# Kernel optimization log

Measured on AMD Instinct MI355X. Metric: run time of the kernel, lower is better.

## Reference

```python
import jax, jax.numpy as jnp
import numpy as np

CH = 256
HEADS = 4
RED = 8  # SE reduction on 2*CH channels


def _conv2d(x, w, pad):
    # x: [b,c,h,w], w: [o,i,kh,kw]
    return jax.lax.conv_general_dilated(
        x, w, window_strides=(1, 1), padding=[(pad, pad), (pad, pad)],
        dimension_numbers=('NCHW', 'OIHW', 'NCHW'))


def setup_inputs() -> dict:
    key = jax.random.key(0)
    ks = jax.random.split(key, 12)
    b, c, h, w = 4, CH, 64, 64
    c2 = 2 * c
    s = 0.02
    inp = {
        'color_feat': jax.random.normal(ks[0], (b, c, h, w), jnp.float32),
        'gray_feat': jax.random.normal(ks[1], (b, c, h, w), jnp.float32),
        'Wq': jax.random.normal(ks[2], (c, c), jnp.float32) * s,
        'Wk': jax.random.normal(ks[3], (c, c), jnp.float32) * s,
        'Wv': jax.random.normal(ks[4], (c, c), jnp.float32) * s,
        'Wproj': jax.random.normal(ks[5], (c, c), jnp.float32) * s,
        'ca_w1': jax.random.normal(ks[6], (c2 // RED, c2), jnp.float32) * s,
        'ca_w2': jax.random.normal(ks[7], (c2, c2 // RED), jnp.float32) * s,
        'sa_w': jax.random.normal(ks[8], (1, 2, 7, 7), jnp.float32) * s,
        'fuse_w': jax.random.normal(ks[9], (c, c2, 3, 3), jnp.float32) * s,
        'bn_gamma': jnp.ones((c,), jnp.float32),
        'bn_beta': jnp.zeros((c,), jnp.float32),
        'bn_mean': jnp.zeros((c,), jnp.float32),
        'bn_var': jnp.ones((c,), jnp.float32),
    }
    return inp


def reference(color_feat, gray_feat, Wq, Wk, Wv, Wproj, ca_w1, ca_w2,
              sa_w, fuse_w, bn_gamma, bn_beta, bn_mean, bn_var):
    b, c, h, w = color_feat.shape
    nh = HEADS
    d = c // nh
    scale = d ** -0.5

    def heads(x, W):
        # 1x1 conv then split heads: [b,c,h,w] -> [b,nh,hw,d]
        y = jnp.einsum('bchw,oc->bohw', x, W)
        return y.reshape(b, nh, d, h * w).transpose(0, 1, 3, 2)

    q = heads(color_feat, Wq)
    k = heads(gray_feat, Wk)
    v = heads(gray_feat, Wv)

    attn = jax.nn.softmax(jnp.einsum('bnid,bnjd->bnij', q, k) * scale, axis=-1)
    out = jnp.einsum('bnij,bnjd->bnid', attn, v)
    out = out.transpose(0, 1, 3, 2).reshape(b, c, h, w)
    out = jnp.einsum('bchw,oc->bohw', out, Wproj)

    cat = jnp.concatenate([out, gray_feat], axis=1)  # [b,2c,h,w]

    # Channel attention (SE with shared MLP on avg- and max-pooled vectors)
    def mlp(z):
        return jax.nn.relu(z @ ca_w1.T) @ ca_w2.T
    avg = cat.mean(axis=(2, 3))
    mx = cat.max(axis=(2, 3))
    wch = jax.nn.sigmoid(mlp(avg) + mlp(mx))[:, :, None, None]
    cat = cat * wch

    # Spatial attention: channel-mean/max -> 7x7 conv -> sigmoid gate
    sa_in = jnp.stack([cat.mean(axis=1), cat.max(axis=1)], axis=1)  # [b,2,h,w]
    wsp = jax.nn.sigmoid(_conv2d(sa_in, sa_w, pad=3))
    cat = cat * wsp

    # Fuse: 3x3 conv -> BatchNorm (inference stats) -> LeakyReLU(0.2)
    y = _conv2d(cat, fuse_w, pad=1)
    inv = bn_gamma / jnp.sqrt(bn_var + 1e-5)
    y = (y - bn_mean[None, :, None, None]) * inv[None, :, None, None] + bn_beta[None, :, None, None]
    return jnp.where(y > 0, y, 0.2 * y)
```

## Files before the change

kernel.cpp:

```cpp
#include <hip/hip_runtime.h>
#include <hip/hip_bf16.h>
#include <stdint.h>

#define HW_ 4096

typedef short bf16x8 __attribute__((ext_vector_type(8)));
typedef short short4v __attribute__((ext_vector_type(4)));
typedef short short8v __attribute__((ext_vector_type(8)));
typedef float f32x4 __attribute__((ext_vector_type(4)));
typedef float f32x16 __attribute__((ext_vector_type(16)));
typedef uint32_t u32x4 __attribute__((ext_vector_type(4)));

__device__ inline unsigned short f2bf(float x) {
  uint32_t u = __builtin_bit_cast(uint32_t, x);
  uint32_t r = ((u >> 16) & 1u) + 0x7fffu;
  return (unsigned short)((u + r) >> 16);
}
__device__ inline uint32_t cvt_pk_bf16(float lo, float hi) {
  uint32_t r;
  asm("v_cvt_pk_bf16_f32 %0, %1, %2" : "=v"(r) : "v"(lo), "v"(hi));
  return r;
}
__device__ inline float bf_lo(uint32_t u) { return __builtin_bit_cast(float, u << 16); }
__device__ inline float bf_hi(uint32_t u) { return __builtin_bit_cast(float, u & 0xffff0000u); }
__device__ inline void gld_lds16(const unsigned short* g, unsigned short* l) {
  __builtin_amdgcn_global_load_lds((const __attribute__((address_space(1))) void*)g,
                                   (__attribute__((address_space(3))) void*)l, 16, 0, 0);
}

__global__ __launch_bounds__(256) void xconv_kernel(
    const float* __restrict__ X, unsigned short* __restrict__ Y) {
  const int i = blockIdx.x * 256 + threadIdx.x;
  const int p = i & 4095;
  const int cg = (i >> 12) & 31;
  const int b = i >> 17;
  const float* src = X + ((size_t)b * 256 + cg * 8) * HW_ + p;
  float v[8];
#pragma unroll
  for (int e = 0; e < 8; ++e) v[e] = src[(size_t)e * HW_];
  uint4 o;
  o.x = cvt_pk_bf16(v[0], v[1]);
  o.y = cvt_pk_bf16(v[2], v[3]);
  o.z = cvt_pk_bf16(v[4], v[5]);
  o.w = cvt_pk_bf16(v[6], v[7]);
  *(uint4*)&Y[((size_t)(b * 32 + cg) * HW_ + p) * 8] = o;
}

__global__ __launch_bounds__(256) void prep_kernel(
    const float* __restrict__ Wq, const float* __restrict__ Wk,
    const float* __restrict__ Wv, const float* __restrict__ Wp,
    const float* __restrict__ fw,
    unsigned short* __restrict__ WqB, unsigned short* __restrict__ WkB,
    unsigned short* __restrict__ WvB, unsigned short* __restrict__ WpB,
    unsigned short* __restrict__ wt) {
  const int blk = blockIdx.x;
  if (blk < 128) {
    const int which = blk >> 5;
    const float* W = which == 0 ? Wq : which == 1 ? Wk : which == 2 ? Wv : Wp;
    unsigned short* Y = which == 0 ? WqB : which == 1 ? WkB : which == 2 ? WvB : WpB;
    const int i = (blk & 31) * 256 + threadIdx.x;
    const int o = i & 255;
    const int cg = i >> 8;
    float4 a = *(const float4*)&W[(size_t)o * 256 + cg * 8];
    float4 bq = *(const float4*)&W[(size_t)o * 256 + cg * 8 + 4];
    uint4 ov;
    ov.x = cvt_pk_bf16(a.x, a.y);
    ov.y = cvt_pk_bf16(a.z, a.w);
    ov.z = cvt_pk_bf16(bq.x, bq.y);
    ov.w = cvt_pk_bf16(bq.z, bq.w);
    *(uint4*)&Y[((size_t)cg * 256 + o) * 8] = ov;
  } else {
    const size_t i = (size_t)(blk - 128) * 256 + threadIdx.x;
    const int oc = (int)(i >> 9);
    const int ic = (int)(i & 511);
    const float* src = fw + i * 9;
#pragma unroll
    for (int tap = 0; tap < 9; ++tap)
      wt[((size_t)tap * 256 + oc) * 512 + ic] = f2bf(src[tap]);
  }
}

__global__ __launch_bounds__(256) void gemm_mfma_kernel(
    const unsigned short* __restrict__ Xbf, const unsigned short* __restrict__ Wbf,
    void* __restrict__ Yv, int mode, float oscale) {
  __shared__ unsigned short W_l[32][64][8];
  __shared__ unsigned short X_l[2][2][128][8];
  const int t = threadIdx.x;
  const int w = t >> 6;
  const int l = t & 63;
  const int n = l & 31;
  const int g32 = l >> 5;
  const int p0 = blockIdx.x * 128;
  const int o0 = blockIdx.y * 64;
  const int b = blockIdx.z;
  const int wo = w >> 1, wp = w & 1;
  const unsigned short* Xb = Xbf + (size_t)b * 32 * HW_ * 8;

  for (int i = t; i < 2048; i += 256) {
    const int ksg = i >> 6, oc = i & 63;
    gld_lds16(Wbf + ((size_t)ksg * 256 + o0 + oc) * 8, &W_l[0][0][0] + (size_t)i * 8);
  }
  {
    const int gg = t >> 7, pp = t & 127;
    gld_lds16(Xb + ((size_t)gg * HW_ + p0 + pp) * 8, &X_l[0][0][0][0] + (size_t)t * 8);
  }
  f32x16 acc[2] = {};
  int buf = 0;
  for (int ks = 0; ks < 16; ++ks) {
    asm volatile("s_waitcnt vmcnt(0)" ::: "memory");
    __syncthreads();
    if (ks < 15) {
      const int gg = t >> 7, pp = t & 127;
      gld_lds16(Xb + ((size_t)((ks + 1) * 2 + gg) * HW_ + p0 + pp) * 8,
                &X_l[buf ^ 1][0][0][0] + (size_t)t * 8);
    }
    bf16x8 af = *(const bf16x8*)&W_l[ks * 2 + g32][wo * 32 + n][0];
    bf16x8 b0 = *(const bf16x8*)&X_l[buf][g32][wp * 64 + n][0];
    bf16x8 b1 = *(const bf16x8*)&X_l[buf][g32][wp * 64 + 32 + n][0];
    acc[0] = __builtin_amdgcn_mfma_f32_32x32x16_bf16(af, b0, acc[0], 0, 0, 0);
    acc[1] = __builtin_amdgcn_mfma_f32_32x32x16_bf16(af, b1, acc[1], 0, 0, 0);
    buf ^= 1;
  }

  if (mode == 1) {
    unsigned short* Y = (unsigned short*)Yv;
    const size_t bh = (size_t)b * 4 + blockIdx.y;
#pragma unroll
    for (int pf = 0; pf < 2; ++pf) {
      const int p = p0 + wp * 64 + pf * 32 + n;
      unsigned short* dst = Y + (bh * HW_ + p) * 64 + wo * 32 + 4 * g32;
#pragma unroll
      for (int q = 0; q < 4; ++q) {
        uint2 uu;
        uu.x = cvt_pk_bf16(acc[pf][q * 4 + 0] * oscale, acc[pf][q * 4 + 1] * oscale);
        uu.y = cvt_pk_bf16(acc[pf][q * 4 + 2] * oscale, acc[pf][q * 4 + 3] * oscale);
        *(uint2*)&dst[8 * q] = uu;
      }
    }
  } else if (mode == 2) {
    unsigned short* Y = (unsigned short*)Yv;
#pragma unroll
    for (int pf = 0; pf < 2; ++pf) {
      const int p = p0 + wp * 64 + pf * 32 + n;
#pragma unroll
      for (int r = 0; r < 16; ++r) {
        const int m = (r & 3) + 8 * (r >> 2) + 4 * g32;
        Y[((size_t)b * 256 + o0 + wo * 32 + m) * HW_ + p] = f2bf(acc[pf][r]);
      }
    }
  } else {
    unsigned short* Y = (unsigned short*)Yv;
    const int cgb = (o0 + wo * 32) >> 3;
#pragma unroll
    for (int pf = 0; pf < 2; ++pf) {
      const int p = p0 + wp * 64 + pf * 32 + n;
#pragma unroll
      for (int q = 0; q < 4; ++q) {
        uint2 uu;
        uu.x = cvt_pk_bf16(acc[pf][q * 4 + 0], acc[pf][q * 4 + 1]);
        uu.y = cvt_pk_bf16(acc[pf][q * 4 + 2], acc[pf][q * 4 + 3]);
        *(uint2*)&Y[((size_t)(b * 32 + cgb + q) * HW_ + p) * 8 + 4 * g32] = uu;
      }
    }
  }
}

#define ATTN_STAGE(SB)                                                       \
  {                                                                          \
    gld_lds16(gKp, kst + (SB) * 4096);                                       \
    gld_lds16(gKp + 8 * 64, kst + (SB) * 4096 + 512);                        \
    gld_lds16(gVp, vst + (SB) * 4096);                                       \
    gld_lds16(gVp + (size_t)8 * HW_, vst + (SB) * 4096 + 512);               \
    gKp += 4096;                                                             \
    gVp += 64;                                                               \
  }

#define ATTN_COMPUTE(BUF)                                                    \
  {                                                                          \
    f32x4 accS[2][4];                                                        \
    _Pragma("unroll") for (int jt = 0; jt < 4; ++jt) {                       \
      bf16x8 kf0 = *(const bf16x8*)&k_l[(BUF) * 4096 + jt * 1024 + ko0];     \
      bf16x8 kf1 = *(const bf16x8*)&k_l[(BUF) * 4096 + jt * 1024 + ko1];     \
      _Pragma("unroll") for (int qt = 0; qt < 2; ++qt) {                     \
        f32x4 s0 = __builtin_amdgcn_mfma_f32_16x16x32_bf16(kf0, qf[qt][0], zero4, 0, 0, 0); \
        accS[qt][jt] = __builtin_amdgcn_mfma_f32_16x16x32_bf16(kf1, qf[qt][1], s0, 0, 0, 0); \
      }                                                                      \
    }                                                                        \
    uint32_t pwu[2][2][4];                                                   \
    _Pragma("unroll") for (int qt = 0; qt < 2; ++qt) {                       \
      float rs = 0.f;                                                        \
      _Pragma("unroll") for (int jt = 0; jt < 4; ++jt) {                     \
        const float e0 = __builtin_amdgcn_exp2f(accS[qt][jt][0]);            \
        const float e1 = __builtin_amdgcn_exp2f(accS[qt][jt][1]);            \
        const float e2 = __builtin_amdgcn_exp2f(accS[qt][jt][2]);            \
        const float e3 = __builtin_amdgcn_exp2f(accS[qt][jt][3]);            \
        rs += (e0 + e1) + (e2 + e3);                                         \
        pwu[qt][jt >> 1][(jt & 1) * 2 + 0] = cvt_pk_bf16(e0, e1);            \
        pwu[qt][jt >> 1][(jt & 1) * 2 + 1] = cvt_pk_bf16(e2, e3);            \
      }                                                                      \
      l_r[qt] += rs;                                                         \
    }                                                                        \
    bf16x8 pf[2][2];                                                         \
    _Pragma("unroll") for (int qt = 0; qt < 2; ++qt)                         \
    _Pragma("unroll") for (int kb = 0; kb < 2; ++kb) {                       \
      u32x4 tmp = {pwu[qt][kb][0], pwu[qt][kb][1], pwu[qt][kb][2], pwu[qt][kb][3]}; \
      pf[qt][kb] = __builtin_bit_cast(bf16x8, tmp);                          \
    }                                                                        \
    _Pragma("unroll") for (int dt = 0; dt < 4; ++dt) {                       \
      union { short4v h[2]; bf16x8 v8; } vv0, vv1;                           \
      vv0.h[0] = *(const short4v*)&v_l[(BUF) * 4096 + dt * 1024 + vo00];     \
      vv0.h[1] = *(const short4v*)&v_l[(BUF) * 4096 + dt * 1024 + vo01];     \
      vv1.h[0] = *(const short4v*)&v_l[(BUF) * 4096 + dt * 1024 + vo10];     \
      vv1.h[1] = *(const short4v*)&v_l[(BUF) * 4096 + dt * 1024 + vo11];     \
      accO[0][dt] = __builtin_amdgcn_mfma_f32_16x16x32_bf16(vv0.v8, pf[0][0], accO[0][dt], 0, 0, 0); \
      accO[1][dt] = __builtin_amdgcn_mfma_f32_16x16x32_bf16(vv0.v8, pf[1][0], accO[1][dt], 0, 0, 0); \
      accO[0][dt] = __builtin_amdgcn_mfma_f32_16x16x32_bf16(vv1.v8, pf[0][1], accO[0][dt], 0, 0, 0); \
      accO[1][dt] = __builtin_amdgcn_mfma_f32_16x16x32_bf16(vv1.v8, pf[1][1], accO[1][dt], 0, 0, 0); \
    }                                                                        \
  }

#define ATTN_PHASE(B, SB, VMSTR, DOST)                                       \
  asm volatile("s_waitcnt " VMSTR ::: "memory");                             \
  __builtin_amdgcn_s_barrier();                                              \
  if (DOST) { ATTN_STAGE(SB) }                                               \
  ATTN_COMPUTE(B)

__global__ __launch_bounds__(256) void attn_mfma_kernel(
    const unsigned short* __restrict__ Qb, const unsigned short* __restrict__ Kb,
    const unsigned short* __restrict__ Vb, unsigned short* __restrict__ Abf) {
  __shared__ unsigned short k_l[4 * 4096];
  __shared__ unsigned short v_l[4 * 4096];
  const int t = threadIdx.x;
  const int w = t >> 6;
  const int l = t & 63;
  const int g = l >> 4;
  const int c = l & 15;
  const int bid = blockIdx.x;
  const int gidx = (bid & 7) * 64 + (bid >> 3);
  const int bn = gidx >> 5;
  const int q0 = (gidx & 31) * 128 + w * 32;

  bf16x8 qf[2][2];
#pragma unroll
  for (int qt = 0; qt < 2; ++qt)
#pragma unroll
    for (int dh = 0; dh < 2; ++dh)
      qf[qt][dh] = *(const bf16x8*)&Qb[((size_t)bn * HW_ + q0 + qt * 16 + c) * 64 + dh * 32 + g * 8];

  const int sw = c & 7;
  const int ko0 = c * 64 + ((g ^ sw) * 8);
  const int ko1 = c * 64 + (((4 + g) ^ sw) * 8);
  const int vb_ = c * 64 + (g & 1) * 4;
  const int gh = g >> 1;
  const int vo00 = vb_ + (((0 + gh) ^ sw) * 8);
  const int vo01 = vb_ + (((2 + gh) ^ sw) * 8);
  const int vo10 = vb_ + (((4 + gh) ^ sw) * 8);
  const int vo11 = vb_ + (((6 + gh) ^ sw) * 8);

  const int srow = 16 * w + (l >> 3);
  const int schunk = (l & 7) ^ ((l >> 3) & 7);
  const unsigned short* gKp = Kb + ((size_t)bn * HW_ + srow) * 64 + schunk * 8;
  const unsigned short* gVp = Vb + ((size_t)bn * 64 + srow) * HW_ + schunk * 8;
  unsigned short* kst = k_l + w * 1024;
  unsigned short* vst = v_l + w * 1024;

  f32x4 accO[2][4] = {};
  float l_r[2] = {0.f, 0.f};
  const f32x4 zero4 = {0.f, 0.f, 0.f, 0.f};

  ATTN_STAGE(0)
  ATTN_STAGE(1)

  for (int t4 = 0; t4 < 15; ++t4) {
    ATTN_PHASE(0, 2, "vmcnt(4)", 1)
    ATTN_PHASE(1, 3, "vmcnt(4)", 1)
    ATTN_PHASE(2, 0, "vmcnt(4)", 1)
    ATTN_PHASE(3, 1, "vmcnt(4)", 1)
  }
  ATTN_PHASE(0, 2, "vmcnt(4)", 1)
  ATTN_PHASE(1, 3, "vmcnt(4)", 1)
  ATTN_PHASE(2, 0, "vmcnt(4)", 0)
  ATTN_PHASE(3, 0, "vmcnt(0)", 0)

  const int head = bn & 3;
  const int bb = bn >> 2;
#pragma unroll
  for (int qt = 0; qt < 2; ++qt) {
    float s = l_r[qt];
    s += __shfl_xor(s, 16);
    s += __shfl_xor(s, 32);
    const float inv = 1.0f / s;
    const int p = q0 + qt * 16 + c;
#pragma unroll
    for (int dt = 0; dt < 4; ++dt) {
      uint2 uu;
      uu.x = cvt_pk_bf16(accO[qt][dt][0] * inv, accO[qt][dt][1] * inv);
      uu.y = cvt_pk_bf16(accO[qt][dt][2] * inv, accO[qt][dt][3] * inv);
      const int cg = head * 8 + dt * 2 + (g >> 1);
      *(uint2*)&Abf[((size_t)(bb * 32 + cg) * HW_ + p) * 8 + (g & 1) * 4] = uu;
    }
  }
}

__global__ __launch_bounds__(256) void pool_kernel(
    const unsigned short* __restrict__ Pbf, const unsigned short* __restrict__ Gbf,
    float* __restrict__ psum, float* __restrict__ pmaxH) {
  const int cg = blockIdx.x;
  const int b = blockIdx.y;
  const int half = blockIdx.z;
  const int t = threadIdx.x;
  const unsigned short* P = Pbf + ((size_t)(b * 32 + cg) * HW_ + half * 2048) * 8;
  const unsigned short* G = Gbf + ((size_t)(b * 32 + cg) * HW_ + half * 2048) * 8;
  float s[16], m[16];
#pragma unroll
  for (int i = 0; i < 16; ++i) { s[i] = 0.f; m[i] = -1e30f; }
  for (int p = t; p < 2048; p += 256) {
    uint4 a = *(const uint4*)&P[(size_t)p * 8];
    uint4 gg = *(const uint4*)&G[(size_t)p * 8];
    const uint32_t ua[4] = {a.x, a.y, a.z, a.w};
    const uint32_t ug[4] = {gg.x, gg.y, gg.z, gg.w};
#pragma unroll
    for (int q = 0; q < 4; ++q) {
      const float a0 = bf_lo(ua[q]), a1 = bf_hi(ua[q]);
      const float g0 = bf_lo(ug[q]), g1 = bf_hi(ug[q]);
      s[q * 2] += a0; s[q * 2 + 1] += a1;
      m[q * 2] = fmaxf(m[q * 2], a0); m[q * 2 + 1] = fmaxf(m[q * 2 + 1], a1);
      s[8 + q * 2] += g0; s[8 + q * 2 + 1] += g1;
      m[8 + q * 2] = fmaxf(m[8 + q * 2], g0); m[8 + q * 2 + 1] = fmaxf(m[8 + q * 2 + 1], g1);
    }
  }
#pragma unroll
  for (int i = 0; i < 16; ++i)
#pragma unroll
    for (int off = 1; off < 64; off <<= 1) {
      s[i] += __shfl_xor(s[i], off);
      m[i] = fmaxf(m[i], __shfl_xor(m[i], off));
    }
  __shared__ float red[4][32];
  const int wv = t >> 6;
  if ((t & 63) == 0) {
#pragma unroll
    for (int i = 0; i < 16; ++i) { red[wv][i] = s[i]; red[wv][16 + i] = m[i]; }
  }
  __syncthreads();
  if (t < 32) {
    const float v0 = red[0][t], v1 = red[1][t], v2 = red[2][t], v3 = red[3][t];
    if (t < 16) {
      const int ch = (t < 8) ? cg * 8 + t : 256 + cg * 8 + (t - 8);
      psum[half * 2048 + b * 512 + ch] = v0 + v1 + v2 + v3;
    } else {
      const int i = t - 16;
      const int ch = (i < 8) ? cg * 8 + i : 256 + cg * 8 + (i - 8);
      pmaxH[half * 2048 + b * 512 + ch] = fmaxf(fmaxf(v0, v1), fmaxf(v2, v3));
    }
  }
}

__global__ __launch_bounds__(256) void se_kernel(
    const float* __restrict__ psum, const float* __restrict__ pmaxH,
    const float* __restrict__ w1, const float* __restrict__ w2,
    float* __restrict__ wch) {
  const int b = blockIdx.x;
  const int t = threadIdx.x;
  __shared__ float za[512], zm[512], hs[64];
  za[t] = (psum[b * 512 + t] + psum[2048 + b * 512 + t]) * (1.f / 4096.f);
  za[256 + t] = (psum[b * 512 + 256 + t] + psum[2048 + b * 512 + 256 + t]) * (1.f / 4096.f);
  zm[t] = fmaxf(pmaxH[b * 512 + t], pmaxH[2048 + b * 512 + t]);
  zm[256 + t] = fmaxf(pmaxH[b * 512 + 256 + t], pmaxH[2048 + b * 512 + 256 + t]);
  __syncthreads();
  if (t < 64) {
    float ha = 0.f, hm = 0.f;
    for (int c = 0; c < 512; ++c) {
      const float w = w1[t * 512 + c];
      ha += w * za[c];
      hm += w * zm[c];
    }
    hs[t] = fmaxf(ha, 0.f) + fmaxf(hm, 0.f);
  }
  __syncthreads();
  for (int o = t; o < 512; o += 256) {
    float acc = 0.f;
#pragma unroll
    for (int hh = 0; hh < 64; ++hh) acc += hs[hh] * w2[o * 64 + hh];
    wch[b * 512 + o] = 1.f / (1.f + __expf(-acc));
  }
}

__global__ __launch_bounds__(256) void sa_reduce_kernel(
    const unsigned short* __restrict__ Pbf, const unsigned short* __restrict__ Gbf,
    const float* __restrict__ wch, float* __restrict__ sa_in) {
  const int b = blockIdx.y;
  const int t = threadIdx.x;
  const int px = t & 63;
  const int sl = t >> 6;
  const int p = blockIdx.x * 64 + px;
  __shared__ float wl[512];
  __shared__ float sred[4][64], mred[4][64];
  wl[t] = wch[b * 512 + t];
  wl[256 + t] = wch[b * 512 + 256 + t];
  __syncthreads();
  float s = 0.f, mx = -1e30f;
#pragma unroll 4
  for (int k = 0; k < 16; ++k) {
    const int chunk = sl * 16 + k;
    const unsigned short* src = (chunk < 32)
        ? &Pbf[((size_t)(b * 32 + chunk) * HW_ + p) * 8]
        : &Gbf[((size_t)(b * 32 + (chunk - 32)) * HW_ + p) * 8];
    uint4 a = *(const uint4*)src;
    const uint32_t u[4] = {a.x, a.y, a.z, a.w};
#pragma unroll
    for (int q = 0; q < 4; ++q) {
      const float v0 = bf_lo(u[q]) * wl[chunk * 8 + q * 2];
      const float v1 = bf_hi(u[q]) * wl[chunk * 8 + q * 2 + 1];
      s += v0 + v1;
      mx = fmaxf(mx, fmaxf(v0, v1));
    }
  }
  sred[sl][px] = s;
  mred[sl][px] = mx;
  __syncthreads();
  if (sl == 0) {
    const float S = sred[0][px] + sred[1][px] + sred[2][px] + sred[3][px];
    const float M = fmaxf(fmaxf(mred[0][px], mred[1][px]), fmaxf(mred[2][px], mred[3][px]));
    sa_in[((size_t)b * 2 + 0) * HW_ + p] = S * (1.f / 512.f);
    sa_in[((size_t)b * 2 + 1) * HW_ + p] = M;
  }
}

__global__ __launch_bounds__(256) void sa_conv_kernel(
    const float* __restrict__ sa_in, const float* __restrict__ sa_w,
    float* __restrict__ wsp) {
  const int b = blockIdx.y;
  const int t = threadIdx.x;
  __shared__ float pl[2][64][64];
  __shared__ float wl[98];
  for (int e = t; e < 8192; e += 256) ((float*)pl)[e] = sa_in[(size_t)b * 8192 + e];
  if (t < 98) wl[t] = sa_w[t];
  __syncthreads();
  const int pix = blockIdx.x * 256 + t;
  const int y = pix >> 6, x = pix & 63;
  float acc = 0.f;
#pragma unroll
  for (int ic = 0; ic < 2; ++ic)
#pragma unroll
    for (int ky = 0; ky < 7; ++ky) {
      const int yy = y + ky - 3;
      if (yy < 0 || yy > 63) continue;
#pragma unroll
      for (int kx = 0; kx < 7; ++kx) {
        const int xx = x + kx - 3;
        if (xx < 0 || xx > 63) continue;
        acc += pl[ic][yy][xx] * wl[ic * 49 + ky * 7 + kx];
      }
    }
  wsp[(size_t)b * HW_ + pix] = 1.f / (1.f + __expf(-acc));
}

__global__ __launch_bounds__(256) void gate_kernel(
    const unsigned short* __restrict__ Pbf, const unsigned short* __restrict__ Gbf,
    const float* __restrict__ wch, const float* __restrict__ wsp,
    unsigned short* __restrict__ catg) {
  const int yp = blockIdx.x;
  const int b = blockIdx.y;
  const int t = threadIdx.x;
  unsigned short* rowp = catg + ((size_t)b * 66 + yp) * 80 * 512;
  if (yp == 0 || yp == 65) {
    short8v z = {};
    for (int m = t; m < 5120; m += 256) *(short8v*)&rowp[m * 8] = z;
    return;
  }
  const int y = yp - 1;
  __shared__ unsigned short tile[64][512];
  __shared__ float wchl[512];
  __shared__ float wspl[64];
  for (int e = t; e < 512; e += 256) wchl[e] = wch[b * 512 + e];
  if (t < 64) wspl[t] = wsp[(size_t)b * HW_ + y * 64 + t];
  {
    short8v z = {};
    for (int m = t; m < 1024; m += 256) {
      const int col = m >> 6;
      const int xi = (col < 8) ? col : (col + 64);
      *(short8v*)&rowp[(size_t)xi * 512 + (m & 63) * 8] = z;
    }
  }
  __syncthreads();
  const int x = t & 63;
  const int cs = t >> 6;
  const float wx = wspl[x];
#pragma unroll
  for (int k = 0; k < 16; ++k) {
    const int chunk = cs * 16 + k;
    const unsigned short* src = (chunk < 32)
        ? &Pbf[((size_t)(b * 32 + chunk) * HW_ + y * 64 + x) * 8]
        : &Gbf[((size_t)(b * 32 + (chunk - 32)) * HW_ + y * 64 + x) * 8];
    uint4 a = *(const uint4*)src;
    const uint32_t u[4] = {a.x, a.y, a.z, a.w};
    uint32_t o[4];
#pragma unroll
    for (int q = 0; q < 4; ++q) {
      const float lo = bf_lo(u[q]) * wchl[chunk * 8 + q * 2] * wx;
      const float hi = bf_hi(u[q]) * wchl[chunk * 8 + q * 2 + 1] * wx;
      o[q] = cvt_pk_bf16(lo, hi);
    }
    uint4 ov = {o[0], o[1], o[2], o[3]};
    *(uint4*)&tile[x][(chunk ^ (x & 7)) * 8] = ov;
  }
  __syncthreads();
#pragma unroll
  for (int j = 0; j < 16; ++j) {
    const int xi = (t >> 6) + 4 * j;
    const int c8 = t & 63;
    uint4 v = *(const uint4*)&tile[xi][(c8 ^ (xi & 7)) * 8];
    *(uint4*)&rowp[(size_t)(xi + 8) * 512 + c8 * 8] = v;
  }
}

__global__ __launch_bounds__(256) void fuse_mfma_kernel(
    const unsigned short* __restrict__ catg, const unsigned short* __restrict__ wt,
    const float* __restrict__ bn_g, const float* __restrict__ bn_b,
    const float* __restrict__ bn_m, const float* __restrict__ bn_v,
    float* __restrict__ out) {
  __shared__ unsigned short X_l[2][6][2][80][8];
  __shared__ unsigned short W_l[2][9][2][32][8];
  __shared__ float invl[32], shl[32];
  const int t = threadIdx.x;
  const int w = t >> 6;
  const int l = t & 63;
  const int n = l & 31;
  const int g = l >> 5;
  const int i = blockIdx.x;
  const int xcd = i & 7, slot = i >> 3;
  const int ocB = slot & 7;
  const int yb = xcd + 8 * (slot >> 3);
  const int y0 = (yb & 15) * 4;
  const int o0 = ocB * 32;
  const int b = yb >> 4;

  if (t < 32) {
    const float iv = bn_g[o0 + t] * rsqrtf(bn_v[o0 + t] + 1e-5f);
    invl[t] = iv;
    shl[t] = bn_b[o0 + t] - bn_m[o0 + t] * iv;
  }

  const unsigned short* catb = catg + ((size_t)b * 66 + y0) * 80 * 512;

  auto stageX = [&](int bi, int ic0) {
    for (int wc = w; wc < 15; wc += 4) {
      const int m = wc * 64 + l;
      const int lr = m / 160;
      const int rem = m - lr * 160;
      const int half = rem / 80;
      const int xi = rem - half * 80;
      gld_lds16(catb + ((size_t)lr * 80 + xi) * 512 + ic0 + half * 8,
                &X_l[bi][0][0][0][0] + (size_t)wc * 512);
    }
  };
  auto stageW = [&](int bi, int ic0) {
    for (int wc = w; wc < 9; wc += 4) {
      const int m = wc * 64 + l;
      const int tap = m >> 6;
      const int rem = m & 63;
      const int half = rem >> 5;
      const int oc = rem & 31;
      gld_lds16(wt + ((size_t)tap * 256 + o0 + oc) * 512 + ic0 + half * 8,
                &W_l[bi][0][0][0][0] + (size_t)wc * 512);
    }
  };

  f32x16 acc[2] = {};

  stageX(0, 0);
  stageW(0, 0);
  int buf = 0;
  for (int ks = 0; ks < 32; ++ks) {
    asm volatile("s_waitcnt vmcnt(0)" ::: "memory");
    __syncthreads();
    if (ks < 31) {
      stageX(buf ^ 1, (ks + 1) * 16);
      stageW(buf ^ 1, (ks + 1) * 16);
    }
#pragma unroll
    for (int ky = 0; ky < 3; ++ky) {
      const int lr = w + ky;
#pragma unroll
      for (int kx = 0; kx < 3; ++kx) {
        const int tap = ky * 3 + kx;
        bf16x8 a0 = *(const bf16x8*)&W_l[buf][tap][g][n][0];
        bf16x8 b0 = *(const bf16x8*)&X_l[buf][lr][g][n + kx + 7][0];
        bf16x8 b1 = *(const bf16x8*)&X_l[buf][lr][g][32 + n + kx + 7][0];
        acc[0] = __builtin_amdgcn_mfma_f32_32x32x16_bf16(a0, b0, acc[0], 0, 0, 0);
        acc[1] = __builtin_amdgcn_mfma_f32_32x32x16_bf16(a0, b1, acc[1], 0, 0, 0);
      }
    }
    buf ^= 1;
  }

#pragma unroll
  for (int pf = 0; pf < 2; ++pf)
#pragma unroll
    for (int r = 0; r < 16; ++r) {
      const int row = (r & 3) + 8 * (r >> 2) + 4 * g;
      const float yv = acc[pf][r] * invl[row] + shl[row];
      const float ov = yv > 0.f ? yv : 0.2f * yv;
      out[((size_t)b * 256 + o0 + row) * HW_ + (size_t)(y0 + w) * 64 + pf * 32 + n] = ov;
    }
}

extern "C" void kernel_launch(void* const* d_in, const int* in_sizes, int n_in,
                              void* d_out, int out_size, void* d_ws, size_t ws_size,
                              hipStream_t stream) {
  const float* color  = (const float*)d_in[0];
  const float* gray   = (const float*)d_in[1];
  const float* Wq     = (const float*)d_in[2];
  const float* Wk     = (const float*)d_in[3];
  const float* Wv     = (const float*)d_in[4];
  const float* Wproj  = (const float*)d_in[5];
  const float* ca_w1  = (const float*)d_in[6];
  const float* ca_w2  = (const float*)d_in[7];
  const float* sa_w   = (const float*)d_in[8];
  const float* fuse_w = (const float*)d_in[9];
  const float* bn_g   = (const float*)d_in[10];
  const float* bn_b   = (const float*)d_in[11];
  const float* bn_m   = (const float*)d_in[12];
  const float* bn_v   = (const float*)d_in[13];
  float* out = (float*)d_out;

  char* ws = (char*)d_ws;
  unsigned short* Cbf = (unsigned short*)(ws);
  unsigned short* Gbf = (unsigned short*)(ws + (8u << 20));
  unsigned short* Qbf = (unsigned short*)(ws + (16u << 20));
  unsigned short* Kbf = (unsigned short*)(ws + (24u << 20));
  unsigned short* Vbf = (unsigned short*)(ws + (32u << 20));
  unsigned short* Abf = (unsigned short*)(ws);
  unsigned short* Pbf = (unsigned short*)(ws + (16u << 20));
  unsigned short* catg = (unsigned short*)(ws + (24u << 20));
  unsigned short* WqB = (unsigned short*)(ws + (45u << 20));
  unsigned short* WkB = WqB + 65536;
  unsigned short* WvB = WkB + 65536;
  unsigned short* WpB = WvB + 65536;
  unsigned short* Wt  = (unsigned short*)(ws + (45u << 20) + (1u << 19));
  float* psum  = (float*)(ws + (48u << 20));
  float* pmaxH = psum + 4096;
  float* wch   = pmaxH + 4096;
  float* sa_in = wch + 2048;
  float* wsp   = sa_in + 32768;
  (void)in_sizes; (void)n_in; (void)out_size; (void)ws_size;

  const float qscale = 0.125f * 1.44269504f;

  prep_kernel<<<dim3(640), 256, 0, stream>>>(Wq, Wk, Wv, Wproj, fuse_w,
                                             WqB, WkB, WvB, WpB, Wt);
  xconv_kernel<<<dim3(2048), 256, 0, stream>>>(color, Cbf);
  xconv_kernel<<<dim3(2048), 256, 0, stream>>>(gray, Gbf);

  dim3 g_gemm(32, 4, 4);
  gemm_mfma_kernel<<<g_gemm, 256, 0, stream>>>(Cbf, WqB, Qbf, 1, qscale);
  gemm_mfma_kernel<<<g_gemm, 256, 0, stream>>>(Gbf, WkB, Kbf, 1, 1.0f);
  gemm_mfma_kernel<<<g_gemm, 256, 0, stream>>>(Gbf, WvB, Vbf, 2, 1.0f);
  attn_mfma_kernel<<<dim3(512), 256, 0, stream>>>(Qbf, Kbf, Vbf, Abf);
  gemm_mfma_kernel<<<g_gemm, 256, 0, stream>>>(Abf, WpB, Pbf, 3, 1.0f);

  pool_kernel<<<dim3(32, 4, 2), 256, 0, stream>>>(Pbf, Gbf, psum, pmaxH);
  se_kernel<<<dim3(4), 256, 0, stream>>>(psum, pmaxH, ca_w1, ca_w2, wch);
  sa_reduce_kernel<<<dim3(64, 4), 256, 0, stream>>>(Pbf, Gbf, wch, sa_in);
  sa_conv_kernel<<<dim3(16, 4), 256, 0, stream>>>(sa_in, sa_w, wsp);
  gate_kernel<<<dim3(66, 4), 256, 0, stream>>>(Pbf, Gbf, wch, wsp, catg);
  fuse_mfma_kernel<<<dim3(512), 256, 0, stream>>>(catg, Wt, bn_g, bn_b, bn_m, bn_v, out);
}
```

Measured before the change: 253.4 us.

## Switch attention to 32x32 MFMA tiles and deepen GEMM LDS pipeline

The attention kernel now uses 32x32x16 bf16 MFMAs instead of 16x16x32 ones. It recomputes the K/V LDS offsets and the P fragment packing to match, which reduces instruction count and LDS reads per FLOP. The 1x1-conv GEMM moves from double to quad buffering of X tiles with partial vmcnt waits, so it no longer drains all loads every step. A combined waitcnt+barrier macro with a sched_barrier is also added. The trade-off is higher register pressure from the f32x16 accumulators and exp arrays, plus the risk of subtle layout mismatches in the fragment mapping.

```diff
diff --git a/kernel.cpp b/kernel.cpp
--- a/kernel.cpp
+++ b/kernel.cpp
@@ -27,6 +27,10 @@
   __builtin_amdgcn_global_load_lds((const __attribute__((address_space(1))) void*)g,
                                    (__attribute__((address_space(3))) void*)l, 16, 0, 0);
 }
+
+#define WAIT_BARRIER(VMSTR)                                                  \
+  asm volatile("s_waitcnt " VMSTR "\n\ts_barrier" ::: "memory");             \
+  __builtin_amdgcn_sched_barrier(0);
 
 __global__ __launch_bounds__(256) void xconv_kernel(
     const float* __restrict__ X, unsigned short* __restrict__ Y) {
@@ -80,11 +84,23 @@
   }
 }
 
+#define GSTAGE(KS, BUF)                                                       \
+  gld_lds16(Xb + ((size_t)((KS) * 2 + (t >> 7)) * HW_ + p0 + (t & 127)) * 8,  \
+            &X_l[BUF][0][0][0] + (size_t)t * 8);
+#define GCOMP(KS)                                                             \
+  {                                                                           \
+    bf16x8 af = *(const bf16x8*)&W_l[(KS) * 2 + g32][wo * 32 + n][0];         \
+    bf16x8 b0 = *(const bf16x8*)&X_l[(KS) & 3][g32][wp * 64 + n][0];          \
+    bf16x8 b1 = *(const bf16x8*)&X_l[(KS) & 3][g32][wp * 64 + 32 + n][0];     \
+    acc[0] = __builtin_amdgcn_mfma_f32_32x32x16_bf16(af, b0, acc[0], 0, 0, 0);\
+    acc[1] = __builtin_amdgcn_mfma_f32_32x32x16_bf16(af, b1, acc[1], 0, 0, 0);\
+  }
+
 __global__ __launch_bounds__(256) void gemm_mfma_kernel(
     const unsigned short* __restrict__ Xbf, const unsigned short* __restrict__ Wbf,
     void* __restrict__ Yv, int mode, float oscale) {
   __shared__ unsigned short W_l[32][64][8];
-  __shared__ unsigned short X_l[2][2][128][8];
+  __shared__ unsigned short X_l[4][2][128][8];
   const int t = threadIdx.x;
   const int w = t >> 6;
   const int l = t & 63;
@@ -96,31 +112,28 @@
   const int wo = w >> 1, wp = w & 1;
   const unsigned short* Xb = Xbf + (size_t)b * 32 * HW_ * 8;
 
-  for (int i = t; i < 2048; i += 256) {
-    const int ksg = i >> 6, oc = i & 63;
-    gld_lds16(Wbf + ((size_t)ksg * 256 + o0 + oc) * 8, &W_l[0][0][0] + (size_t)i * 8);
-  }
-  {
-    const int gg = t >> 7, pp = t & 127;
-    gld_lds16(Xb + ((size_t)gg * HW_ + p0 + pp) * 8, &X_l[0][0][0][0] + (size_t)t * 8);
-  }
+#pragma unroll
+  for (int j = 0; j < 8; ++j) {
+    const int i = j * 256 + t;
+    gld_lds16(Wbf + ((size_t)(i >> 6) * 256 + o0 + (i & 63)) * 8,
+              &W_l[0][0][0] + (size_t)i * 8);
+  }
+  GSTAGE(0, 0)
+  GSTAGE(1, 1)
+  GSTAGE(2, 2)
+
   f32x16 acc[2] = {};
-  int buf = 0;
-  for (int ks = 0; ks < 16; ++ks) {
-    asm volatile("s_waitcnt vmcnt(0)" ::: "memory");
-    __syncthreads();
-    if (ks < 15) {
-      const int gg = t >> 7, pp = t & 127;
-      gld_lds16(Xb + ((size_t)((ks + 1) * 2 + gg) * HW_ + p0 + pp) * 8,
-                &X_l[buf ^ 1][0][0][0] + (size_t)t * 8);
-    }
-    bf16x8 af = *(const bf16x8*)&W_l[ks * 2 + g32][wo * 32 + n][0];
-    bf16x8 b0 = *(const bf16x8*)&X_l[buf][g32][wp * 64 + n][0];
-    bf16x8 b1 = *(const bf16x8*)&X_l[buf][g32][wp * 64 + 32 + n][0];
-    acc[0] = __builtin_amdgcn_mfma_f32_32x32x16_bf16(af, b0, acc[0], 0, 0, 0);
-    acc[1] = __builtin_amdgcn_mfma_f32_32x32x16_bf16(af, b1, acc[1], 0, 0, 0);
-    buf ^= 1;
-  }
+  for (int ks = 0; ks < 13; ++ks) {
+    WAIT_BARRIER("vmcnt(2)")
+    GSTAGE(ks + 3, (ks + 3) & 3)
+    GCOMP(ks)
+  }
+  WAIT_BARRIER("vmcnt(2)")
+  GCOMP(13)
+  WAIT_BARRIER("vmcnt(1)")
+  GCOMP(14)
+  WAIT_BARRIER("vmcnt(0)")
+  GCOMP(15)
 
   if (mode == 1) {
     unsigned short* Y = (unsigned short*)Yv;
@@ -177,51 +190,52 @@
 
 #define ATTN_COMPUTE(BUF)                                                    \
   {                                                                          \
-    f32x4 accS[2][4];                                                        \
-    _Pragma("unroll") for (int jt = 0; jt < 4; ++jt) {                       \
-      bf16x8 kf0 = *(const bf16x8*)&k_l[(BUF) * 4096 + jt * 1024 + ko0];     \
-      bf16x8 kf1 = *(const bf16x8*)&k_l[(BUF) * 4096 + jt * 1024 + ko1];     \
-      _Pragma("unroll") for (int qt = 0; qt < 2; ++qt) {                     \
-        f32x4 s0 = __builtin_amdgcn_mfma_f32_16x16x32_bf16(kf0, qf[qt][0], zero4, 0, 0, 0); \
-        accS[qt][jt] = __builtin_amdgcn_mfma_f32_16x16x32_bf16(kf1, qf[qt][1], s0, 0, 0, 0); \
-      }                                                                      \
+    f32x16 aS0 = zero16, aS1 = zero16;                                       \
+    _Pragma("unroll") for (int s = 0; s < 4; ++s) {                          \
+      bf16x8 kf0 = *(const bf16x8*)&k_l[(BUF) * 4096 + rowKA + kox[s]];      \
+      bf16x8 kf1 = *(const bf16x8*)&k_l[(BUF) * 4096 + rowKB + kox[s]];      \
+      aS0 = __builtin_amdgcn_mfma_f32_32x32x16_bf16(kf0, qf[s], aS0, 0, 0, 0); \
+      aS1 = __builtin_amdgcn_mfma_f32_32x32x16_bf16(kf1, qf[s], aS1, 0, 0, 0); \
     }                                                                        \
-    uint32_t pwu[2][2][4];                                                   \
-    _Pragma("unroll") for (int qt = 0; qt < 2; ++qt) {                       \
-      float rs = 0.f;                                                        \
-      _Pragma("unroll") for (int jt = 0; jt < 4; ++jt) {                     \
-        const float e0 = __builtin_amdgcn_exp2f(accS[qt][jt][0]);            \
-        const float e1 = __builtin_amdgcn_exp2f(accS[qt][jt][1]);            \
-        const float e2 = __builtin_amdgcn_exp2f(accS[qt][jt][2]);            \
-        const float e3 = __builtin_amdgcn_exp2f(accS[qt][jt][3]);            \
-        rs += (e0 + e1) + (e2 + e3);                                         \
-        pwu[qt][jt >> 1][(jt & 1) * 2 + 0] = cvt_pk_bf16(e0, e1);            \
-        pwu[qt][jt >> 1][(jt & 1) * 2 + 1] = cvt_pk_bf16(e2, e3);            \
-      }                                                                      \
-      l_r[qt] += rs;                                                         \
+    float ex0[16], ex1[16];                                                  \
+    float rs = 0.f;                                                          \
+    _Pragma("unroll") for (int r = 0; r < 16; ++r) {                         \
+      ex0[r] = __builtin_amdgcn_exp2f(aS0[r]);                               \
+      ex1[r] = __builtin_amdgcn_exp2f(aS1[r]);                               \
+      rs += ex0[r] + ex1[r];                                                 \
     }                                                                        \
-    bf16x8 pf[2][2];                                                         \
-    _Pragma("unroll") for (int qt = 0; qt < 2; ++qt)                         \
-    _Pragma("unroll") for (int kb = 0; kb < 2; ++kb) {                       \
-      u32x4 tmp = {pwu[qt][kb][0], pwu[qt][kb][1], pwu[qt][kb][2], pwu[qt][kb][3]}; \
-      pf[qt][kb] = __builtin_bit_cast(bf16x8, tmp);                          \
+    l_r += rs;                                                               \
+    union { u32x4 u4; bf16x8 v8; } pA, pB, pC, pD;                           \
+    pA.u4 = (u32x4){cvt_pk_bf16(ex0[0], ex0[1]), cvt_pk_bf16(ex0[2], ex0[3]),    \
+                    cvt_pk_bf16(ex0[4], ex0[5]), cvt_pk_bf16(ex0[6], ex0[7])};   \
+    pB.u4 = (u32x4){cvt_pk_bf16(ex0[8], ex0[9]), cvt_pk_bf16(ex0[10], ex0[11]),  \
+                    cvt_pk_bf16(ex0[12], ex0[13]), cvt_pk_bf16(ex0[14], ex0[15])};\
+    pC.u4 = (u32x4){cvt_pk_bf16(ex1[0], ex1[1]), cvt_pk_bf16(ex1[2], ex1[3]),    \
+                    cvt_pk_bf16(ex1[4], ex1[5]), cvt_pk_bf16(ex1[6], ex1[7])};   \
+    pD.u4 = (u32x4){cvt_pk_bf16(ex1[8], ex1[9]), cvt_pk_bf16(ex1[10], ex1[11]),  \
+                    cvt_pk_bf16(ex1[12], ex1[13]), cvt_pk_bf16(ex1[14], ex1[15])};\
+    _Pragma("unroll") for (int dh = 0; dh < 2; ++dh) {                       \
+      const int rw = (BUF) * 4096 + (dh * 32 + n) * 64;                      \
+      union { short4v h2[2]; bf16x8 v8; } v0, v1, v2, v3;                    \
+      v0.h2[0] = *(const short4v*)&v_l[rw + voA0];                           \
+      v0.h2[1] = *(const short4v*)&v_l[rw + voA1];                           \
+      v1.h2[0] = *(const short4v*)&v_l[rw + voB0];                           \
+      v1.h2[1] = *(const short4v*)&v_l[rw + voB1];                           \
+      v2.h2[0] = *(const short4v*)&v_l[rw + voC0];                           \
+      v2.h2[1] = *(const short4v*)&v_l[rw + voC1];                           \
+      v3.h2[0] = *(const short4v*)&v_l[rw + voD0];                           \
+      v3.h2[1] = *(const short4v*)&v_l[rw + voD1];                           \
+      f32x16 ac = accO[dh];                                                  \
+      ac = __builtin_amdgcn_mfma_f32_32x32x16_bf16(v0.v8, pA.v8, ac, 0, 0, 0); \
+      ac = __builtin_amdgcn_mfma_f32_32x32x16_bf16(v1.v8, pB.v8, ac, 0, 0, 0); \
+      ac = __builtin_amdgcn_mfma_f32_32x32x16_bf16(v2.v8, pC.v8, ac, 0, 0, 0); \
+      ac = __builtin_amdgcn_mfma_f32_32x32x16_bf16(v3.v8, pD.v8, ac, 0, 0, 0); \
+      accO[dh] = ac;                                                         \
     }                                                                        \
-    _Pragma("unroll") for (int dt = 0; dt < 4; ++dt) {                       \
-      union { short4v h[2]; bf16x8 v8; } vv0, vv1;                           \
-      vv0.h[0] = *(const short4v*)&v_l[(BUF) * 4096 + dt * 1024 + vo00];     \
-      vv0.h[1] = *(const short4v*)&v_l[(BUF) * 4096 + dt * 1024 + vo01];     \
-      vv1.h[0] = *(const short4v*)&v_l[(BUF) * 4096 + dt * 1024 + vo10];     \
-      vv1.h[1] = *(const short4v*)&v_l[(BUF) * 4096 + dt * 1024 + vo11];     \
-      accO[0][dt] = __builtin_amdgcn_mfma_f32_16x16x32_bf16(vv0.v8, pf[0][0], accO[0][dt], 0, 0, 0); \
-      accO[1][dt] = __builtin_amdgcn_mfma_f32_16x16x32_bf16(vv0.v8, pf[1][0], accO[1][dt], 0, 0, 0); \
-      accO[0][dt] = __builtin_amdgcn_mfma_f32_16x16x32_bf16(vv1.v8, pf[0][1], accO[0][dt], 0, 0, 0); \
-      accO[1][dt] = __builtin_amdgcn_mfma_f32_16x16x32_bf16(vv1.v8, pf[1][1], accO[1][dt], 0, 0, 0); \
-    }                                                                        \
   }
 
 #define ATTN_PHASE(B, SB, VMSTR, DOST)                                       \
-  asm volatile("s_waitcnt " VMSTR ::: "memory");                             \
-  __builtin_amdgcn_s_barrier();                                              \
+  WAIT_BARRIER(VMSTR)                                                        \
   if (DOST) { ATTN_STAGE(SB) }                                               \
   ATTN_COMPUTE(B)
 
@@ -233,29 +247,29 @@
   const int t = threadIdx.x;
   const int w = t >> 6;
   const int l = t & 63;
-  const int g = l >> 4;
-  const int c = l & 15;
+  const int n = l & 31;
+  const int h = l >> 5;
   const int bid = blockIdx.x;
   const int gidx = (bid & 7) * 64 + (bid >> 3);
   const int bn = gidx >> 5;
   const int q0 = (gidx & 31) * 128 + w * 32;
 
-  bf16x8 qf[2][2];
-#pragma unroll
-  for (int qt = 0; qt < 2; ++qt)
-#pragma unroll
-    for (int dh = 0; dh < 2; ++dh)
-      qf[qt][dh] = *(const bf16x8*)&Qb[((size_t)bn * HW_ + q0 + qt * 16 + c) * 64 + dh * 32 + g * 8];
-
-  const int sw = c & 7;
-  const int ko0 = c * 64 + ((g ^ sw) * 8);
-  const int ko1 = c * 64 + (((4 + g) ^ sw) * 8);
-  const int vb_ = c * 64 + (g & 1) * 4;
-  const int gh = g >> 1;
-  const int vo00 = vb_ + (((0 + gh) ^ sw) * 8);
-  const int vo01 = vb_ + (((2 + gh) ^ sw) * 8);
-  const int vo10 = vb_ + (((4 + gh) ^ sw) * 8);
-  const int vo11 = vb_ + (((6 + gh) ^ sw) * 8);
+  bf16x8 qf[4];
+#pragma unroll
+  for (int s = 0; s < 4; ++s)
+    qf[s] = *(const bf16x8*)&Qb[((size_t)bn * HW_ + q0 + n) * 64 + s * 16 + h * 8];
+
+  const int n7 = n & 7;
+  const int rowKA = n * 64;
+  const int rowKB = (32 + n) * 64;
+  int kox[4];
+#pragma unroll
+  for (int s = 0; s < 4; ++s) kox[s] = ((2 * s + h) ^ n7) * 8;
+  const int h4 = 4 * h;
+  const int voA0 = ((0 ^ n7) * 8) + h4, voA1 = ((1 ^ n7) * 8) + h4;
+  const int voB0 = ((2 ^ n7) * 8) + h4, voB1 = ((3 ^ n7) * 8) + h4;
+  const int voC0 = ((4 ^ n7) * 8) + h4, voC1 = ((5 ^ n7) * 8) + h4;
+  const int voD0 = ((6 ^ n7) * 8) + h4, voD1 = ((7 ^ n7) * 8) + h4;
 
   const int srow = 16 * w + (l >> 3);
   const int schunk = (l & 7) ^ ((l >> 3) & 7);
@@ -264,9 +278,9 @@
   unsigned short* kst = k_l + w * 1024;
   unsigned short* vst = v_l + w * 1024;
 
-  f32x4 accO[2][4] = {};
-  float l_r[2] = {0.f, 0.f};
-  const f32x4 zero4 = {0.f, 0.f, 0.f, 0.f};
+  f32x16 accO[2] = {};
+  float l_r = 0.f;
+  const f32x16 zero16 = {};
 
   ATTN_STAGE(0)
   ATTN_STAGE(1)
@@ -284,22 +298,19 @@
 
   const int head = bn & 3;
   const int bb = bn >> 2;
-#pragma unroll
-  for (int qt = 0; qt < 2; ++qt) {
-    float s = l_r[qt];
-    s += __shfl_xor(s, 16);
-    s += __shfl_xor(s, 32);
-    const float inv = 1.0f / s;
-    const int p = q0 + qt * 16 + c;
-#pragma unroll
-    for (int dt = 0; dt < 4; ++dt) {
+  const float lsum = l_r + __shfl_xor(l_r, 32);
+  const float inv = 1.0f / lsum;
+  const int pcol = q0 + n;
+#pragma unroll
+  for (int dh = 0; dh < 2; ++dh)
+#pragma unroll
+    for (int k4 = 0; k4 < 4; ++k4) {
       uint2 uu;
-      uu.x = cvt_pk_bf16(accO[qt][dt][0] * inv, accO[qt][dt][1] * inv);
-      uu.y = cvt_pk_bf16(accO[qt][dt][2] * inv, accO[qt][dt][3] * inv);
-      const int cg = head * 8 + dt * 2 + (g >> 1);
-      *(uint2*)&Abf[((size_t)(bb * 32 + cg) * HW_ + p) * 8 + (g & 1) * 4] = uu;
-    }
-  }
+      uu.x = cvt_pk_bf16(accO[dh][k4 * 4 + 0] * inv, accO[dh][k4 * 4 + 1] * inv);
+      uu.y = cvt_pk_bf16(accO[dh][k4 * 4 + 2] * inv, accO[dh][k4 * 4 + 3] * inv);
+      const int cg = head * 8 + dh * 4 + k4;
+      *(uint2*)&Abf[((size_t)(bb * 32 + cg) * HW_ + pcol) * 8 + h4] = uu;
+    }
 }
 
 __global__ __launch_bounds__(256) void pool_kernel(
```

Result: slower. 260.9 us (+3.0%).
